# Optimization experiments

Hardware: AMD Instinct MI355X
Metric: run time of the kernel (lower is better)

## Reference

```python
import jax, jax.numpy as jnp
import numpy as np

NUM_CLASSES = 2
THRESH = 0.5        # overlap_thresh
NEGPOS = 3          # neg:pos ratio
VAR = (0.1, 0.2)    # cfg['variance']
B, P, O = 64, 32768, 50


def point_form(p):
    # center-size [cx,cy,w,h] -> corner [xmin,ymin,xmax,ymax]
    return jnp.concatenate([p[:, :2] - p[:, 2:] * 0.5, p[:, :2] + p[:, 2:] * 0.5], axis=1)


def iou(a, b):
    # a [O,4], b [P,4] corner form -> [O,P]
    lt = jnp.maximum(a[:, None, :2], b[None, :, :2])
    rb = jnp.minimum(a[:, None, 2:], b[None, :, 2:])
    wh = jnp.clip(rb - lt, 0.0, None)
    inter = wh[..., 0] * wh[..., 1]
    area_a = ((a[:, 2] - a[:, 0]) * (a[:, 3] - a[:, 1]))[:, None]
    area_b = ((b[:, 2] - b[:, 0]) * (b[:, 3] - b[:, 1]))[None, :]
    return inter / (area_a + area_b - inter)


def encode(matched, priors_cs):
    g_cxcy = ((matched[:, :2] + matched[:, 2:]) * 0.5 - priors_cs[:, :2]) / (VAR[0] * priors_cs[:, 2:])
    g_wh = jnp.log((matched[:, 2:] - matched[:, :2]) / priors_cs[:, 2:]) / VAR[1]
    return jnp.concatenate([g_cxcy, g_wh], axis=1)


def match_one(truths, labels, priors_cs, priors_pt):
    ovl = iou(truths, priors_pt)                # [O,P]
    best_prior_idx = jnp.argmax(ovl, axis=1)    # [O] best prior per GT
    best_truth_ovl = jnp.max(ovl, axis=0)       # [P]
    best_truth_idx = jnp.argmax(ovl, axis=0)    # [P]
    best_truth_ovl = best_truth_ovl.at[best_prior_idx].set(2.0)
    best_truth_idx = best_truth_idx.at[best_prior_idx].set(jnp.arange(truths.shape[0]))
    matched = truths[best_truth_idx]            # [P,4]
    conf = jnp.where(best_truth_ovl < THRESH, 0, labels[best_truth_idx])
    return encode(matched, priors_cs), conf


def reference(arm_loc, arm_conf, odm_loc, odm_conf, priors, targets):
    loc_data, conf_data = arm_loc, arm_conf    # use_ARM=False -> ARM branch
    num, num_priors = loc_data.shape[0], loc_data.shape[1]
    truths = targets[..., :4]
    labels = (targets[..., 4] >= 0).astype(jnp.int32)   # num_classes == 2 binarization
    priors_pt = point_form(priors)
    loc_t, conf_t = jax.vmap(lambda t, l: match_one(t, l, priors, priors_pt))(truths, labels)
    loc_t = jax.lax.stop_gradient(loc_t)
    conf_t = jax.lax.stop_gradient(conf_t)
    pos = conf_t > 0                             # [B,P]
    # localization: smooth L1, summed over positives
    d = loc_data - loc_t
    ad = jnp.abs(d)
    sl1 = jnp.where(ad < 1.0, 0.5 * d * d, ad - 0.5)
    loss_l = jnp.sum(sl1 * pos[..., None].astype(loc_data.dtype))
    # per-prior conf loss for hard negative mining
    lse = jax.nn.logsumexp(conf_data, axis=-1)   # [B,P]
    picked = jnp.take_along_axis(conf_data, conf_t[..., None], axis=-1)[..., 0]
    lc = lse - picked                            # NLL per prior
    lc_mine = jnp.where(pos, 0.0, lc)            # zero positives before ranking
    order = jnp.argsort(-lc_mine, axis=1)        # descending sort
    rank = jnp.argsort(order, axis=1)            # rank of each prior
    num_pos = jnp.sum(pos, axis=1, keepdims=True)            # [B,1]
    num_neg = jnp.minimum(NEGPOS * num_pos, num_priors - 1)
    neg = rank < num_neg
    sel = (pos | neg).astype(conf_data.dtype)
    loss_c = jnp.sum(lc * sel)
    N = jnp.sum(num_pos).astype(loc_data.dtype)
    return loss_l / N, loss_c / N


def setup_inputs():
    key = jax.random.key(0)
    ks = jax.random.split(key, 8)
    arm_loc = jax.random.normal(ks[0], (B, P, 4), jnp.float32)
    arm_conf = jax.random.normal(ks[1], (B, P, NUM_CLASSES), jnp.float32)
    odm_loc = jax.random.normal(ks[2], (B, P, 4), jnp.float32)
    odm_conf = jax.random.normal(ks[3], (B, P, NUM_CLASSES), jnp.float32)
    # priors in center-size form
    p_cxcy = jax.random.uniform(ks[4], (P, 2), jnp.float32, 0.05, 0.95)
    p_wh = jax.random.uniform(ks[5], (P, 2), jnp.float32, 0.05, 0.5)
    priors = jnp.concatenate([p_cxcy, p_wh], axis=1)
    # GT boxes in corner form with valid extents, labels >= 0
    t_cxcy = jax.random.uniform(ks[6], (B, O, 2), jnp.float32, 0.2, 0.8)
    t_wh = jax.random.uniform(ks[7], (B, O, 2), jnp.float32, 0.05, 0.3)
    boxes = jnp.concatenate([t_cxcy - t_wh * 0.5, t_cxcy + t_wh * 0.5], axis=-1)
    targets = jnp.concatenate([boxes, jnp.ones((B, O, 1), jnp.float32)], axis=-1)
    return {"arm_loc": arm_loc, "arm_conf": arm_conf, "odm_loc": odm_loc,
            "odm_conf": odm_conf, "priors": priors, "targets": targets}
```

## Files before the change

kernel.cpp:

```cpp
#include <hip/hip_runtime.h>
#include <cstdint>

#pragma clang fp contract(off)

#define BB 64
#define PP 32768
#define OO 50
#define THRESH_F 0.5f
#define VAR0 0.1f
#define VAR1 0.2f
#define NEGPOS_I 3
#define SS 32
#define T1 4
#define NB0 2048
#define NB12 1024
#define NCELL 1024

typedef unsigned long long u64;

__device__ __forceinline__ unsigned mpart4(unsigned x) {
    x = (x | (x << 2)) & 0x33u;
    x = (x | (x << 1)) & 0x55u;
    return x;
}
__device__ __forceinline__ int cell_of(float4 pr) {
    int xb = (int)(pr.x * 16.0f); xb = xb < 0 ? 0 : (xb > 15 ? 15 : xb);
    int yb = (int)(pr.y * 16.0f); yb = yb < 0 ? 0 : (yb > 15 ? 15 : yb);
    float s = fmaxf(pr.z, pr.w);
    int wc = s < 0.275f ? 0 : (s < 0.368f ? 1 : (s < 0.44f ? 2 : 3));
    return wc * 256 + (int)(mpart4((unsigned)xb) | (mpart4((unsigned)yb) << 1));
}

__global__ void k_zero(float4* __restrict__ dst, int n4) {
    int i = blockIdx.x * blockDim.x + threadIdx.x;
    if (i < n4) dst[i] = make_float4(0.f, 0.f, 0.f, 0.f);
}

__global__ void k_phist(const float4* __restrict__ pri, int* __restrict__ cnt) {
    int p = blockIdx.x * 1024 + threadIdx.x * 4;
    for (int j = 0; j < 4; ++j)
        atomicAdd(&cnt[cell_of(pri[p + j])], 1);
}

__global__ void __launch_bounds__(256)
k_pss(const float4* __restrict__ pri, const int* __restrict__ cnt,
      int* __restrict__ cursor, int* __restrict__ perm, int* __restrict__ iperm) {
    __shared__ int sc[256];
    __shared__ int sbase[NCELL];
    int tid = threadIdx.x;
    int a[4]; int s = 0;
    for (int i = 0; i < 4; ++i) { a[i] = cnt[tid * 4 + i]; s += a[i]; }
    sc[tid] = s; __syncthreads();
    for (int off = 1; off < 256; off <<= 1) {
        int v = (tid >= off) ? sc[tid - off] : 0;
        __syncthreads(); sc[tid] += v; __syncthreads();
    }
    int excl = sc[tid] - s;
    for (int i = 0; i < 4; ++i) { sbase[tid * 4 + i] = excl; excl += a[i]; }
    __syncthreads();
    int p = blockIdx.x * 1024 + tid * 4;
    for (int j = 0; j < 4; ++j) {
        int c = cell_of(pri[p + j]);
        int pos = sbase[c] + atomicAdd(&cursor[c], 1);
        perm[pos] = p + j;
        iperm[p + j] = pos;
    }
}

#define DPP_MAX(x, ctrl, rmask)                                              \
    {                                                                        \
        int _o = __float_as_int(x);                                          \
        x = fmaxf(x, __int_as_float(__builtin_amdgcn_update_dpp(             \
                _o, _o, (ctrl), (rmask), 0xf, false)));                      \
    }
#define DPP_MINF(x, ctrl, rmask)                                             \
    {                                                                        \
        int _o = __float_as_int(x);                                          \
        x = fminf(x, __int_as_float(__builtin_amdgcn_update_dpp(             \
                _o, _o, (ctrl), (rmask), 0xf, false)));                      \
    }
#define WAVE_MAXF(x) { DPP_MAX(x,0x111,0xf); DPP_MAX(x,0x112,0xf); DPP_MAX(x,0x114,0xf); \
                       DPP_MAX(x,0x118,0xf); DPP_MAX(x,0x142,0xa); DPP_MAX(x,0x143,0xc); }
#define WAVE_MINF(x) { DPP_MINF(x,0x111,0xf); DPP_MINF(x,0x112,0xf); DPP_MINF(x,0x114,0xf); \
                       DPP_MINF(x,0x118,0xf); DPP_MINF(x,0x142,0xa); DPP_MINF(x,0x143,0xc); }

__device__ __forceinline__ float sl1enc(const float* __restrict__ tb,
                                        float4 pr, float4 ld) {
    float gx = ((tb[0] + tb[2]) * 0.5f - pr.x) / (VAR0 * pr.z);
    float gy = ((tb[1] + tb[3]) * 0.5f - pr.y) / (VAR0 * pr.w);
    float gw = logf((tb[2] - tb[0]) / pr.z) / VAR1;
    float gh = logf((tb[3] - tb[1]) / pr.w) / VAR1;
    float g[4] = {gx, gy, gw, gh};
    float l[4] = {ld.x, ld.y, ld.z, ld.w};
    float s = 0.f;
    for (int q = 0; q < 4; ++q) {
        float d = l[q] - g[q];
        float ad = fabsf(d);
        s += (ad < 1.0f) ? 0.5f * d * d : ad - 0.5f;
    }
    return s;
}

__global__ void __launch_bounds__(256, 8)
k_ml(const float* __restrict__ priors, const int* __restrict__ perm,
     const float* __restrict__ targets,
     const float* __restrict__ arm_loc, const float* __restrict__ arm_conf,
     float* __restrict__ lcmP, unsigned char* __restrict__ bpiP,
     u64* __restrict__ bpm,
     float* __restrict__ pll, float* __restrict__ pplc, int* __restrict__ pnp) {
    __shared__ float4 trP[OO];
    __shared__ float2 trQ[OO];
    __shared__ float s1[256]; __shared__ float s2[256]; __shared__ int s3[256];
    int b = (blockIdx.x % 8) * 8 + (blockIdx.y % 8);
    int s = (blockIdx.x / 8) + 4 * (blockIdx.y / 8);
    int tid = threadIdx.x;
    if (tid < OO) {
        const float* tb = &targets[(size_t)(b * OO + tid) * 5];
        float x0 = tb[0], y0 = tb[1], x1 = tb[2], y1 = tb[3];
        trP[tid] = make_float4(x0, y0, x1, y1);
        trQ[tid] = make_float2((x1 - x0) * (y1 - y0), tb[4]);
    }
    __syncthreads();

    int p0 = s * (256 * T1) + tid * T1;
    int4 o4 = ((const int4*)perm)[p0 >> 2];
    int o_[T1] = {o4.x, o4.y, o4.z, o4.w};
    int omin = min(min(o_[0], o_[1]), min(o_[2], o_[3]));
    float bx0[T1], by0[T1], bx1[T1], by1[T1], aB[T1];
#pragma unroll
    for (int j = 0; j < T1; ++j) {
        float4 pr = ((const float4*)priors)[o_[j]];
        bx0[j] = pr.x - pr.z * 0.5f; by0[j] = pr.y - pr.w * 0.5f;
        bx1[j] = pr.x + pr.z * 0.5f; by1[j] = pr.y + pr.w * 0.5f;
        aB[j] = (bx1[j] - bx0[j]) * (by1[j] - by0[j]);
    }
    float lx0 = fminf(fminf(bx0[0], bx0[1]), fminf(bx0[2], bx0[3]));
    float ly0 = fminf(fminf(by0[0], by0[1]), fminf(by0[2], by0[3]));
    float lx1 = fmaxf(fmaxf(bx1[0], bx1[1]), fmaxf(bx1[2], bx1[3]));
    float ly1 = fmaxf(fmaxf(by1[0], by1[1]), fmaxf(by1[2], by1[3]));
    WAVE_MINF(lx0); WAVE_MINF(ly0); WAVE_MAXF(lx1); WAVE_MAXF(ly1);
    float wx0 = __int_as_float(__builtin_amdgcn_readlane(__float_as_int(lx0), 63));
    float wy0 = __int_as_float(__builtin_amdgcn_readlane(__float_as_int(ly0), 63));
    float wx1 = __int_as_float(__builtin_amdgcn_readlane(__float_as_int(lx1), 63));
    float wy1 = __int_as_float(__builtin_amdgcn_readlane(__float_as_int(ly1), 63));

    float rbv[T1]; int rbi[T1];
#pragma unroll
    for (int j = 0; j < T1; ++j) { rbv[j] = 0.0f; rbi[j] = 0; }

    for (int t = 0; t < OO; ++t) {
        float4 tP = trP[t];
        if (!(tP.z > wx0 && tP.x < wx1 && tP.w > wy0 && tP.y < wy1)) continue;
        float aA = trQ[t].x;
        float I[T1];
#pragma unroll
        for (int j = 0; j < T1; ++j) {
            float ltx = fmaxf(tP.x, bx0[j]), lty = fmaxf(tP.y, by0[j]);
            float rbx = fminf(tP.z, bx1[j]), rby = fminf(tP.w, by1[j]);
            float wx = fmaxf(rbx - ltx, 0.f), wy = fmaxf(rby - lty, 0.f);
            I[j] = wx * wy;
        }
        bool anyl = (I[0] > 0.f) | (I[1] > 0.f) | (I[2] > 0.f) | (I[3] > 0.f);
        if (__any(anyl)) {
            float cbv = 0.0f; int cbo = omin;
#pragma unroll
            for (int j = 0; j < T1; ++j) {
                float v = I[j] / (aA + aB[j] - I[j]);
                if (v > rbv[j]) { rbv[j] = v; rbi[j] = t; }
                if (v > cbv || (v == cbv && o_[j] < cbo)) { cbv = v; cbo = o_[j]; }
            }
            float x = cbv;
            WAVE_MAXF(x);
            float mvf = __int_as_float(__builtin_amdgcn_readlane(__float_as_int(x), 63));
            if (mvf > 0.0f) {
                u64 msk = __ballot(cbv == mvf);
                int ln = (int)__ffsll((long long)msk) - 1;
                int morig = __builtin_amdgcn_readlane(cbo, ln);
                u64 rest = msk & (msk - 1);
                while (rest) {
                    int l2 = (int)__ffsll((long long)rest) - 1;
                    int o2 = __builtin_amdgcn_readlane(cbo, l2);
                    morig = min(morig, o2);
                    rest &= rest - 1;
                }
                if ((tid & 63) == 0) {
                    u64 pk = ((u64)__float_as_uint(mvf) << 32) | (unsigned)(PP - morig);
                    atomicMax(&bpm[b * OO + t], pk);
                }
            }
        }
    }

    size_t bbase = (size_t)b * PP;
    float ll = 0.0f, plc = 0.0f; int np = 0;
    float outv[4]; unsigned pbyte = 0;
#pragma unroll
    for (int c = 0; c < T1; ++c) {
        int o = o_[c]; size_t bo = bbase + o;
        int ti = rbi[c]; float ov = rbv[c];
        float2 cf = ((const float2*)arm_conf)[bo];
        float c0 = cf.x, c1 = cf.y;
        float m = fmaxf(c0, c1);
        float lse = logf(expf(c0 - m) + expf(c1 - m)) + m;
        bool pos = (ov >= THRESH_F) && (trQ[ti].y >= 0.0f);
        float lc = lse - (pos ? c1 : c0);
        outv[c] = pos ? 0.0f : lc;
        pbyte |= (unsigned)((pos ? 0x80u : 0u) | (unsigned)ti) << (8 * c);
        if (pos) {
            np++; plc += lc;
            float4 pr = ((const float4*)priors)[o];
            float4 ld = ((const float4*)arm_loc)[bo];
            const float4 tv = trP[ti];
            float tb4[4] = {tv.x, tv.y, tv.z, tv.w};
            ll += sl1enc(tb4, pr, ld);
        }
    }
    size_t bq = bbase + p0;
    ((float4*)lcmP)[bq >> 2] = make_float4(outv[0], outv[1], outv[2], outv[3]);
    ((unsigned*)bpiP)[bq >> 2] = pbyte;

    s1[tid] = ll; s2[tid] = plc; s3[tid] = np;
    __syncthreads();
    for (int st = 128; st > 0; st >>= 1) {
        if (tid < st) { s1[tid] += s1[tid+st]; s2[tid] += s2[tid+st]; s3[tid] += s3[tid+st]; }
        __syncthreads();
    }
    if (tid == 0) {
        pll[s * BB + b] = s1[0];
        pplc[s * BB + b] = s2[0];
        pnp[s * BB + b] = s3[0];
    }
}

__global__ void k_fix(const u64* __restrict__ bpm, const float* __restrict__ targets,
                      const float* __restrict__ arm_loc, const float* __restrict__ arm_conf,
                      const float* __restrict__ priors, const int* __restrict__ iperm,
                      const unsigned char* __restrict__ bpiP, float* __restrict__ lcmP,
                      float* __restrict__ pll, float* __restrict__ pplc,
                      int* __restrict__ pnp, int* __restrict__ npb) {
    int b = blockIdx.x, j = threadIdx.x;
    int p = -1;
    if (j < OO) {
        unsigned lo = (unsigned)(bpm[b * OO + j] & 0xFFFFFFFFull);
        p = lo ? (PP - (int)lo) : 0;
    }
    bool w = (j < OO);
    for (int jj = 1; jj < OO; ++jj) {
        int pj = __shfl(p, jj, 64);
        if (jj > j && pj == p) w = false;
    }
    float dll = 0.f, dplc = 0.f; int dnp = 0;
    if (w) {
        int pos_ = iperm[p];
        size_t bq = (size_t)b * PP + pos_;
        size_t bo = (size_t)b * PP + p;
        unsigned char ob = bpiP[bq];
        bool old_pos = (ob & 0x80u) != 0;
        int old_ti = ob & 63;
        float2 cf = ((const float2*)arm_conf)[bo];
        float c0 = cf.x, c1 = cf.y;
        float m = fmaxf(c0, c1);
        float lse = logf(expf(c0 - m) + expf(c1 - m)) + m;
        const float* tbj = &targets[(size_t)(b * OO + j) * 5];
        bool new_pos = (tbj[4] >= 0.0f);
        float new_lcm = new_pos ? 0.0f : (lse - c0);
        lcmP[bq] = new_lcm;
        float4 pr = ((const float4*)priors)[p];
        float4 ld = ((const float4*)arm_loc)[bo];
        if (old_pos) {
            dnp -= 1; dplc -= (lse - c1);
            dll -= sl1enc(&targets[(size_t)(b * OO + old_ti) * 5], pr, ld);
        }
        if (new_pos) {
            dnp += 1; dplc += (lse - c1);
            dll += sl1enc(tbj, pr, ld);
        }
    }
    int myp = (j < SS) ? pnp[j * BB + b] : 0;
    for (int st = 32; st >= 1; st >>= 1) {
        dll += __shfl_down(dll, st, 64);
        dplc += __shfl_down(dplc, st, 64);
        dnp += __shfl_down(dnp, st, 64);
        myp += __shfl_down(myp, st, 64);
    }
    if (j == 0) {
        pll[b] += dll;
        pplc[b] += dplc;
        pnp[b] += dnp;
        npb[b] = myp + dnp;
    }
}

__global__ void __launch_bounds__(256)
k_sel(const float* __restrict__ lcmP, const int* __restrict__ npb,
      float* __restrict__ ssum, int* __restrict__ srem, unsigned* __restrict__ stb) {
    __shared__ int hc[NB0]; __shared__ float hs[NB0];
    __shared__ int sc[256]; __shared__ float sf[256];
    __shared__ int s_chunk, s_r; __shared__ float s_S; __shared__ unsigned s_pref;
    int b = blockIdx.x, tid = threadIdx.x;
    const float4* v4 = (const float4*)(lcmP + (size_t)b * PP);

    {
        for (int i = tid; i < NB0; i += 256) { hc[i] = 0; hs[i] = 0.f; }
        __syncthreads();
        for (int it = 0; it < 32; ++it) {
            float4 x = v4[it * 256 + tid];
            float xs[4] = {x.x, x.y, x.z, x.w};
            for (int c2 = 0; c2 < 4; ++c2) {
                unsigned u = __float_as_uint(xs[c2]);
                atomicAdd(&hc[u >> 20], 1);
                atomicAdd(&hs[u >> 20], xs[c2]);
            }
        }
        __syncthreads();
        int c = 0; float f = 0.f; int base = tid * 8;
        for (int i = 0; i < 8; ++i) { c += hc[base + i]; f += hs[base + i]; }
        sc[tid] = c; sf[tid] = f;
        if (tid == 0) {
            int k = NEGPOS_I * npb[b]; if (k > PP - 1) k = PP - 1;
            s_r = k; s_S = 0.f;
        }
        __syncthreads();
        for (int off = 1; off < 256; off <<= 1) {
            int cv = (tid + off < 256) ? sc[tid + off] : 0;
            float fv = (tid + off < 256) ? sf[tid + off] : 0.f;
            __syncthreads(); sc[tid] += cv; sf[tid] += fv; __syncthreads();
        }
        int r = s_r;
        int nxt = (tid == 255) ? 0 : sc[tid + 1];
        if (sc[tid] >= r && nxt < r) s_chunk = tid;
        __syncthreads();
        if (tid == 0) {
            int ch = s_chunk;
            int r2 = r - ((ch == 255) ? 0 : sc[ch + 1]);
            float S2 = s_S + ((ch == 255) ? 0.f : sf[ch + 1]);
            int binSel = ch * 8;
            for (int i = 7; i >= 0; --i) {
                int bin = ch * 8 + i; int cbn = hc[bin];
                if (r2 <= cbn) { binSel = bin; break; }
                r2 -= cbn; S2 += hs[bin];
            }
            s_pref = (unsigned)binSel; s_r = r2; s_S = S2;
        }
        __syncthreads();
    }
    {
        for (int i = tid; i < NB12; i += 256) { hc[i] = 0; hs[i] = 0.f; }
        __syncthreads();
        unsigned pref = s_pref;
        for (int it = 0; it < 32; ++it) {
            float4 x = v4[it * 256 + tid];
            float xs[4] = {x.x, x.y, x.z, x.w};
            for (int c2 = 0; c2 < 4; ++c2) {
                unsigned u = __float_as_uint(xs[c2]);
                if ((u >> 20) == pref) {
                    atomicAdd(&hc[(u >> 10) & 1023u], 1);
                    atomicAdd(&hs[(u >> 10) & 1023u], xs[c2]);
                }
            }
        }
        __syncthreads();
        int c = 0; float f = 0.f; int base = tid * 4;
        for (int i = 0; i < 4; ++i) { c += hc[base + i]; f += hs[base + i]; }
        sc[tid] = c; sf[tid] = f; __syncthreads();
        for (int off = 1; off < 256; off <<= 1) {
            int cv = (tid + off < 256) ? sc[tid + off] : 0;
            float fv = (tid + off < 256) ? sf[tid + off] : 0.f;
            __syncthreads(); sc[tid] += cv; sf[tid] += fv; __syncthreads();
        }
        int r = s_r;
        int nxt = (tid == 255) ? 0 : sc[tid + 1];
        if (sc[tid] >= r && nxt < r) s_chunk = tid;
        __syncthreads();
        if (tid == 0) {
            int ch = s_chunk;
            int r2 = r - ((ch == 255) ? 0 : sc[ch + 1]);
            float S2 = s_S + ((ch == 255) ? 0.f : sf[ch + 1]);
            int binSel = ch * 4;
            for (int i = 3; i >= 0; --i) {
                int bin = ch * 4 + i; int cbn = hc[bin];
                if (r2 <= cbn) { binSel = bin; break; }
                r2 -= cbn; S2 += hs[bin];
            }
            s_pref = (s_pref << 10) | (unsigned)binSel; s_r = r2; s_S = S2;
        }
        __syncthreads();
    }
    {
        for (int i = tid; i < NB12; i += 256) { hc[i] = 0; hs[i] = 0.f; }
        __syncthreads();
        unsigned pref = s_pref;
        for (int it = 0; it < 32; ++it) {
            float4 x = v4[it * 256 + tid];
            float xs[4] = {x.x, x.y, x.z, x.w};
            for (int c2 = 0; c2 < 4; ++c2) {
                unsigned u = __float_as_uint(xs[c2]);
                if ((u >> 10) == pref) {
                    atomicAdd(&hc[u & 1023u], 1);
                    atomicAdd(&hs[u & 1023u], xs[c2]);
                }
            }
        }
        __syncthreads();
        int c = 0; float f = 0.f; int base = tid * 4;
        for (int i = 0; i < 4; ++i) { c += hc[base + i]; f += hs[base + i]; }
        sc[tid] = c; sf[tid] = f; __syncthreads();
        for (int off = 1; off < 256; off <<= 1) {
            int cv = (tid + off < 256) ? sc[tid + off] : 0;
            float fv = (tid + off < 256) ? sf[tid + off] : 0.f;
            __syncthreads(); sc[tid] += cv; sf[tid] += fv; __syncthreads();
        }
        int r = s_r;
        int nxt = (tid == 255) ? 0 : sc[tid + 1];
        if (sc[tid] >= r && nxt < r) s_chunk = tid;
        __syncthreads();
        if (tid == 0) {
            int ch = s_chunk;
            int r2 = r - ((ch == 255) ? 0 : sc[ch + 1]);
            float S2 = s_S + ((ch == 255) ? 0.f : sf[ch + 1]);
            int binSel = ch * 4;
            for (int i = 3; i >= 0; --i) {
                int bin = ch * 4 + i; int cbn = hc[bin];
                if (r2 <= cbn) { binSel = bin; break; }
                r2 -= cbn; S2 += hs[bin];
            }
            stb[b] = (s_pref << 10) | (unsigned)binSel;
            srem[b] = r2; ssum[b] = S2;
        }
    }
}

__global__ void k_final(const float* __restrict__ pll, const float* __restrict__ pplc,
                        const int* __restrict__ pnp, const float* __restrict__ ssum,
                        const int* __restrict__ srem, const unsigned* __restrict__ stb,
                        float* __restrict__ out) {
    int b = threadIdx.x;
    float ll = 0.f, plc = 0.f; int np = 0;
    for (int s = 0; s < SS; ++s) {
        ll += pll[s * BB + b];
        plc += pplc[s * BB + b];
        np += pnp[s * BB + b];
    }
    float tval = __uint_as_float(stb[b]);
    float cc = plc + ssum[b] + (float)srem[b] * tval;
    for (int s = 32; s > 0; s >>= 1) {
        ll += __shfl_down(ll, s);
        cc += __shfl_down(cc, s);
        np += __shfl_down(np, s);
    }
    if (b == 0) {
        float N = (float)np;
        out[0] = ll / N;
        out[1] = cc / N;
    }
}

extern "C" void kernel_launch(void* const* d_in, const int* in_sizes, int n_in,
                              void* d_out, int out_size, void* d_ws, size_t ws_size,
                              hipStream_t stream) {
    const float* arm_loc  = (const float*)d_in[0];
    const float* arm_conf = (const float*)d_in[1];
    const float* priors   = (const float*)d_in[4];
    const float* targets  = (const float*)d_in[5];
    float* out = (float*)d_out;

    char* w = (char*)d_ws;
    float* lcmP = (float*)w;  w += sizeof(float) * (size_t)BB * PP;
    unsigned char* bpiP = (unsigned char*)w; w += (size_t)BB * PP;
    char* zbase = w;
    int*   cellCnt = (int*)w; w += sizeof(int) * NCELL;
    int*   cursor  = (int*)w; w += sizeof(int) * NCELL;
    u64*   bpm = (u64*)w;    w += sizeof(u64)   * BB * OO;
    size_t zbytes = (size_t)(w - zbase);
    int*   perm  = (int*)w;  w += sizeof(int) * PP;
    int*   iperm = (int*)w;  w += sizeof(int) * PP;
    float* pll  = (float*)w; w += sizeof(float) * BB * SS;
    float* pplc = (float*)w; w += sizeof(float) * BB * SS;
    int*   pnp  = (int*)w;   w += sizeof(int)   * BB * SS;
    int*   npb  = (int*)w;   w += sizeof(int)   * BB;
    int*      srem = (int*)w;      w += sizeof(int) * BB;
    float*    ssum = (float*)w;    w += sizeof(float) * BB;
    unsigned* stb  = (unsigned*)w; w += sizeof(unsigned) * BB;

    int n4 = (int)(zbytes / 16);
    k_zero<<<(n4 + 255) / 256, 256, 0, stream>>>((float4*)zbase, n4);
    k_phist<<<PP / 1024, 256, 0, stream>>>((const float4*)priors, cellCnt);
    k_pss<<<PP / 1024, 256, 0, stream>>>((const float4*)priors, cellCnt, cursor, perm, iperm);
    k_ml<<<dim3(SS, BB), 256, 0, stream>>>(priors, perm, targets, arm_loc, arm_conf,
                                           lcmP, bpiP, bpm, pll, pplc, pnp);
    k_fix<<<BB, 64, 0, stream>>>(bpm, targets, arm_loc, arm_conf, priors, iperm,
                                 bpiP, lcmP, pll, pplc, pnp, npb);
    k_sel<<<BB, 256, 0, stream>>>(lcmP, npb, ssum, srem, stb);
    k_final<<<1, 64, 0, stream>>>(pll, pplc, pnp, ssum, srem, stb, out);
}
```

Measured before the change: 304.5 us.

## Build first radix-select histogram in match kernel and merge prior-sort kernels

The match kernel now builds a per-batch 256-bin histogram (count and sum) over the float exponent bits of the negative-loss values, using shared-memory atomics that are then flushed to global memory. The fix kernel patches this histogram whenever it changes a value. The selection kernel uses the precomputed histogram as its first radix pass, so only two full passes over the loss array remain instead of three, with 12-bit and 11-bit digits. The prior-cell counting sort is merged into a single 1024-thread block kernel, removing one launch and the global atomics, at the cost of running serially on one CU and adding atomic traffic inside the match kernel.

```diff
diff --git a/kernel.cpp b/kernel.cpp
--- a/kernel.cpp
+++ b/kernel.cpp
@@ -12,8 +12,9 @@
 #define NEGPOS_I 3
 #define SS 32
 #define T1 4
-#define NB0 2048
-#define NB12 1024
+#define NB_P0 256
+#define NB_P1 4096
+#define NB_P2 2048
 #define NCELL 1024
 
 typedef unsigned long long u64;
@@ -36,34 +37,30 @@
     if (i < n4) dst[i] = make_float4(0.f, 0.f, 0.f, 0.f);
 }
 
-__global__ void k_phist(const float4* __restrict__ pri, int* __restrict__ cnt) {
-    int p = blockIdx.x * 1024 + threadIdx.x * 4;
-    for (int j = 0; j < 4; ++j)
-        atomicAdd(&cnt[cell_of(pri[p + j])], 1);
-}
-
-__global__ void __launch_bounds__(256)
-k_pss(const float4* __restrict__ pri, const int* __restrict__ cnt,
-      int* __restrict__ cursor, int* __restrict__ perm, int* __restrict__ iperm) {
-    __shared__ int sc[256];
-    __shared__ int sbase[NCELL];
+__global__ void __launch_bounds__(1024)
+k_prep(const float4* __restrict__ pri, int* __restrict__ perm, int* __restrict__ iperm) {
+    __shared__ int cnt[NCELL];
+    __shared__ int tmp[NCELL];
     int tid = threadIdx.x;
-    int a[4]; int s = 0;
-    for (int i = 0; i < 4; ++i) { a[i] = cnt[tid * 4 + i]; s += a[i]; }
-    sc[tid] = s; __syncthreads();
-    for (int off = 1; off < 256; off <<= 1) {
-        int v = (tid >= off) ? sc[tid - off] : 0;
-        __syncthreads(); sc[tid] += v; __syncthreads();
-    }
-    int excl = sc[tid] - s;
-    for (int i = 0; i < 4; ++i) { sbase[tid * 4 + i] = excl; excl += a[i]; }
-    __syncthreads();
-    int p = blockIdx.x * 1024 + tid * 4;
-    for (int j = 0; j < 4; ++j) {
-        int c = cell_of(pri[p + j]);
-        int pos = sbase[c] + atomicAdd(&cursor[c], 1);
-        perm[pos] = p + j;
-        iperm[p + j] = pos;
+    cnt[tid] = 0;
+    __syncthreads();
+    for (int i = 0; i < 32; ++i)
+        atomicAdd(&cnt[cell_of(pri[i * 1024 + tid])], 1);
+    __syncthreads();
+    int v = cnt[tid]; tmp[tid] = v;
+    __syncthreads();
+    for (int off = 1; off < 1024; off <<= 1) {
+        int a = (tid >= off) ? tmp[tid - off] : 0;
+        __syncthreads(); tmp[tid] += a; __syncthreads();
+    }
+    cnt[tid] = tmp[tid] - v;
+    __syncthreads();
+    for (int i = 0; i < 32; ++i) {
+        int p = i * 1024 + tid;
+        int c = cell_of(pri[p]);
+        int pos = atomicAdd(&cnt[c], 1);
+        perm[pos] = p;
+        iperm[p] = pos;
     }
 }
 
@@ -107,9 +104,12 @@
      const float* __restrict__ arm_loc, const float* __restrict__ arm_conf,
      float* __restrict__ lcmP, unsigned char* __restrict__ bpiP,
      u64* __restrict__ bpm,
-     float* __restrict__ pll, float* __restrict__ pplc, int* __restrict__ pnp) {
+     float* __restrict__ pll, float* __restrict__ pplc, int* __restrict__ pnp,
+     int* __restrict__ Hc0, float* __restrict__ Hs0) {
     __shared__ float4 trP[OO];
     __shared__ float2 trQ[OO];
+    __shared__ int   hc[NB_P0];
+    __shared__ float hs[NB_P0];
     __shared__ float s1[256]; __shared__ float s2[256]; __shared__ int s3[256];
     int b = (blockIdx.x % 8) * 8 + (blockIdx.y % 8);
     int s = (blockIdx.x / 8) + 4 * (blockIdx.y / 8);
@@ -120,6 +120,7 @@
         trP[tid] = make_float4(x0, y0, x1, y1);
         trQ[tid] = make_float2((x1 - x0) * (y1 - y0), tb[4]);
     }
+    hc[tid] = 0; hs[tid] = 0.f;
     __syncthreads();
 
     int p0 = s * (256 * T1) + tid * T1;
@@ -206,6 +207,9 @@
         float lc = lse - (pos ? c1 : c0);
         outv[c] = pos ? 0.0f : lc;
         pbyte |= (unsigned)((pos ? 0x80u : 0u) | (unsigned)ti) << (8 * c);
+        unsigned u = __float_as_uint(outv[c]);
+        atomicAdd(&hc[u >> 23], 1);
+        atomicAdd(&hs[u >> 23], outv[c]);
         if (pos) {
             np++; plc += lc;
             float4 pr = ((const float4*)priors)[o];
@@ -219,6 +223,14 @@
     ((float4*)lcmP)[bq >> 2] = make_float4(outv[0], outv[1], outv[2], outv[3]);
     ((unsigned*)bpiP)[bq >> 2] = pbyte;
 
+    __syncthreads();
+    {
+        int cv = hc[tid];
+        if (cv) {
+            atomicAdd(&Hc0[b * NB_P0 + tid], cv);
+            atomicAdd(&Hs0[b * NB_P0 + tid], hs[tid]);
+        }
+    }
     s1[tid] = ll; s2[tid] = plc; s3[tid] = np;
     __syncthreads();
     for (int st = 128; st > 0; st >>= 1) {
@@ -237,7 +249,8 @@
                       const float* __restrict__ priors, const int* __restrict__ iperm,
                       const unsigned char* __restrict__ bpiP, float* __restrict__ lcmP,
                       float* __restrict__ pll, float* __restrict__ pplc,
-                      int* __restrict__ pnp, int* __restrict__ npb) {
+                      int* __restrict__ pnp, int* __restrict__ npb,
+                      int* __restrict__ Hc0, float* __restrict__ Hs0) {
     int b = blockIdx.x, j = threadIdx.x;
     int p = -1;
     if (j < OO) {
@@ -263,8 +276,16 @@
         float lse = logf(expf(c0 - m) + expf(c1 - m)) + m;
         const float* tbj = &targets[(size_t)(b * OO + j) * 5];
         bool new_pos = (tbj[4] >= 0.0f);
+        float old_lcm = lcmP[bq];
         float new_lcm = new_pos ? 0.0f : (lse - c0);
-        lcmP[bq] = new_lcm;
+        unsigned uo = __float_as_uint(old_lcm), un = __float_as_uint(new_lcm);
+        if (uo != un) {
+            atomicAdd(&Hc0[b * NB_P0 + (uo >> 23)], -1);
+            atomicAdd(&Hs0[b * NB_P0 + (uo >> 23)], -old_lcm);
+            atomicAdd(&Hc0[b * NB_P0 + (un >> 23)], 1);
+            atomicAdd(&Hs0[b * NB_P0 + (un >> 23)], new_lcm);
+            lcmP[bq] = new_lcm;
+        }
         float4 pr = ((const float4*)priors)[p];
         float4 ld = ((const float4*)arm_loc)[bo];
         if (old_pos) {
@@ -293,34 +314,101 @@
 
 __global__ void __launch_bounds__(256)
 k_sel(const float* __restrict__ lcmP, const int* __restrict__ npb,
+      const int* __restrict__ Hc0, const float* __restrict__ Hs0,
       float* __restrict__ ssum, int* __restrict__ srem, unsigned* __restrict__ stb) {
-    __shared__ int hc[NB0]; __shared__ float hs[NB0];
+    __shared__ int hc[NB_P1]; __shared__ float hs[NB_P1];
     __shared__ int sc[256]; __shared__ float sf[256];
     __shared__ int s_chunk, s_r; __shared__ float s_S; __shared__ unsigned s_pref;
     int b = blockIdx.x, tid = threadIdx.x;
     const float4* v4 = (const float4*)(lcmP + (size_t)b * PP);
 
     {
-        for (int i = tid; i < NB0; i += 256) { hc[i] = 0; hs[i] = 0.f; }
-        __syncthreads();
+        int c = Hc0[b * NB_P0 + tid];
+        float f = Hs0[b * NB_P0 + tid];
+        sc[tid] = c; sf[tid] = f;
+        if (tid == 0) {
+            int k = NEGPOS_I * npb[b]; if (k > PP - 1) k = PP - 1;
+            s_r = k; s_S = 0.f;
+        }
+        __syncthreads();
+        for (int off = 1; off < 256; off <<= 1) {
+            int cv = (tid + off < 256) ? sc[tid + off] : 0;
+            float fv = (tid + off < 256) ? sf[tid + off] : 0.f;
+            __syncthreads(); sc[tid] += cv; sf[tid] += fv; __syncthreads();
+        }
+        int r = s_r;
+        int nxt = (tid == 255) ? 0 : sc[tid + 1];
+        if (sc[tid] >= r && nxt < r) s_chunk = tid;
+        __syncthreads();
+        if (tid == 0) {
+            int ch = s_chunk;
+            s_pref = (unsigned)ch;
+            s_r = r - ((ch == 255) ? 0 : sc[ch + 1]);
+            s_S = (ch == 255) ? 0.f : sf[ch + 1];
+        }
+        __syncthreads();
+    }
+    {
+        for (int i = tid; i < NB_P1; i += 256) { hc[i] = 0; hs[i] = 0.f; }
+        __syncthreads();
+        unsigned pref = s_pref;
         for (int it = 0; it < 32; ++it) {
             float4 x = v4[it * 256 + tid];
             float xs[4] = {x.x, x.y, x.z, x.w};
             for (int c2 = 0; c2 < 4; ++c2) {
                 unsigned u = __float_as_uint(xs[c2]);
-                atomicAdd(&hc[u >> 20], 1);
-                atomicAdd(&hs[u >> 20], xs[c2]);
+                if ((u >> 23) == pref) {
+                    atomicAdd(&hc[(u >> 11) & 4095u], 1);
+                    atomicAdd(&hs[(u >> 11) & 4095u], xs[c2]);
+                }
+            }
+        }
+        __syncthreads();
+        int c = 0; float f = 0.f; int base = tid * 16;
+        for (int i = 0; i < 16; ++i) { c += hc[base + i]; f += hs[base + i]; }
+        sc[tid] = c; sf[tid] = f; __syncthreads();
+        for (int off = 1; off < 256; off <<= 1) {
+            int cv = (tid + off < 256) ? sc[tid + off] : 0;
+            float fv = (tid + off < 256) ? sf[tid + off] : 0.f;
+            __syncthreads(); sc[tid] += cv; sf[tid] += fv; __syncthreads();
+        }
+        int r = s_r;
+        int nxt = (tid == 255) ? 0 : sc[tid + 1];
+        if (sc[tid] >= r && nxt < r) s_chunk = tid;
+        __syncthreads();
+        if (tid == 0) {
+            int ch = s_chunk;
+            int r2 = r - ((ch == 255) ? 0 : sc[ch + 1]);
+            float S2 = s_S + ((ch == 255) ? 0.f : sf[ch + 1]);
+            int binSel = ch * 16;
+            for (int i = 15; i >= 0; --i) {
+                int bin = ch * 16 + i; int cbn = hc[bin];
+                if (r2 <= cbn) { binSel = bin; break; }
+                r2 -= cbn; S2 += hs[bin];
+            }
+            s_pref = (s_pref << 12) | (unsigned)binSel; s_r = r2; s_S = S2;
+        }
+        __syncthreads();
+    }
+    {
+        for (int i = tid; i < NB_P2; i += 256) { hc[i] = 0; hs[i] = 0.f; }
+        __syncthreads();
+        unsigned pref = s_pref;
+        for (int it = 0; it < 32; ++it) {
+            float4 x = v4[it * 256 + tid];
+            float xs[4] = {x.x, x.y, x.z, x.w};
+            for (int c2 = 0; c2 < 4; ++c2) {
+                unsigned u = __float_as_uint(xs[c2]);
+                if ((u >> 11) == pref) {
+                    atomicAdd(&hc[u & 2047u], 1);
+                    atomicAdd(&hs[u & 2047u], xs[c2]);
+                }
             }
         }
         __syncthreads();
         int c = 0; float f = 0.f; int base = tid * 8;
         for (int i = 0; i < 8; ++i) { c += hc[base + i]; f += hs[base + i]; }
-        sc[tid] = c; sf[tid] = f;
-        if (tid == 0) {
-            int k = NEGPOS_I * npb[b]; if (k > PP - 1) k = PP - 1;
-            s_r = k; s_S = 0.f;
-        }
-        __syncthreads();
+        sc[tid] = c; sf[tid] = f; __syncthreads();
         for (int off = 1; off < 256; off <<= 1) {
             int cv = (tid + off < 256) ? sc[tid + off] : 0;
             float fv = (tid + off < 256) ? sf[tid + off] : 0.f;
@@ -340,91 +428,7 @@
                 if (r2 <= cbn) { binSel = bin; break; }
                 r2 -= cbn; S2 += hs[bin];
             }
-            s_pref = (unsigned)binSel; s_r = r2; s_S = S2;
-        }
-        __syncthreads();
-    }
-    {
-        for (int i = tid; i < NB12; i += 256) { hc[i] = 0; hs[i] = 0.f; }
-        __syncthreads();
-        unsigned pref = s_pref;
-        for (int it = 0; it < 32; ++it) {
-            float4 x = v4[it * 256 + tid];
-            float xs[4] = {x.x, x.y, x.z, x.w};
-            for (int c2 = 0; c2 < 4; ++c2) {
-                unsigned u = __float_as_uint(xs[c2]);
-                if ((u >> 20) == pref) {
-                    atomicAdd(&hc[(u >> 10) & 1023u], 1);
-                    atomicAdd(&hs[(u >> 10) & 1023u], xs[c2]);
-                }
-            }
-        }
-        __syncthreads();
-        int c = 0; float f = 0.f; int base = tid * 4;
-        for (int i = 0; i < 4; ++i) { c += hc[base + i]; f += hs[base + i]; }
-        sc[tid] = c; sf[tid] = f; __syncthreads();
-        for (int off = 1; off < 256; off <<= 1) {
-            int cv = (tid + off < 256) ? sc[tid + off] : 0;
-            float fv = (tid + off < 256) ? sf[tid + off] : 0.f;
-            __syncthreads(); sc[tid] += cv; sf[tid] += fv; __syncthreads();
-        }
-        int r = s_r;
-        int nxt = (tid == 255) ? 0 : sc[tid + 1];
-        if (sc[tid] >= r && nxt < r) s_chunk = tid;
-        __syncthreads();
-        if (tid == 0) {
-            int ch = s_chunk;
-            int r2 = r - ((ch == 255) ? 0 : sc[ch + 1]);
-            float S2 = s_S + ((ch == 255) ? 0.f : sf[ch + 1]);
-            int binSel = ch * 4;
-            for (int i = 3; i >= 0; --i) {
-                int bin = ch * 4 + i; int cbn = hc[bin];
-                if (r2 <= cbn) { binSel = bin; break; }
-                r2 -= cbn; S2 += hs[bin];
-            }
-            s_pref = (s_pref << 10) | (unsigned)binSel; s_r = r2; s_S = S2;
-        }
-        __syncthreads();
-    }
-    {
-        for (int i = tid; i < NB12; i += 256) { hc[i] = 0; hs[i] = 0.f; }
-        __syncthreads();
-        unsigned pref = s_pref;
-        for (int it = 0; it < 32; ++it) {
-            float4 x = v4[it * 256 + tid];
-            float xs[4] = {x.x, x.y, x.z, x.w};
-            for (int c2 = 0; c2 < 4; ++c2) {
-                unsigned u = __float_as_uint(xs[c2]);
-                if ((u >> 10) == pref) {
-                    atomicAdd(&hc[u & 1023u], 1);
-                    atomicAdd(&hs[u & 1023u], xs[c2]);
-                }
-            }
-        }
-        __syncthreads();
-        int c = 0; float f = 0.f; int base = tid * 4;
-        for (int i = 0; i < 4; ++i) { c += hc[base + i]; f += hs[base + i]; }
-        sc[tid] = c; sf[tid] = f; __syncthreads();
-        for (int off = 1; off < 256; off <<= 1) {
-            int cv = (tid + off < 256) ? sc[tid + off] : 0;
-            float fv = (tid + off < 256) ? sf[tid + off] : 0.f;
-            __syncthreads(); sc[tid] += cv; sf[tid] += fv; __syncthreads();
-        }
-        int r = s_r;
-        int nxt = (tid == 255) ? 0 : sc[tid + 1];
-        if (sc[tid] >= r && nxt < r) s_chunk = tid;
-        __syncthreads();
-        if (tid == 0) {
-            int ch = s_chunk;
-            int r2 = r - ((ch == 255) ? 0 : sc[ch + 1]);
-            float S2 = s_S + ((ch == 255) ? 0.f : sf[ch + 1]);
-            int binSel = ch * 4;
-            for (int i = 3; i >= 0; --i) {
-                int bin = ch * 4 + i; int cbn = hc[bin];
-                if (r2 <= cbn) { binSel = bin; break; }
-                r2 -= cbn; S2 += hs[bin];
-            }
-            stb[b] = (s_pref << 10) | (unsigned)binSel;
+            stb[b] = (s_pref << 11) | (unsigned)binSel;
             srem[b] = r2; ssum[b] = S2;
         }
     }
@@ -468,8 +472,8 @@
     float* lcmP = (float*)w;  w += sizeof(float) * (size_t)BB * PP;
     unsigned char* bpiP = (unsigned char*)w; w += (size_t)BB * PP;
     char* zbase = w;
-    int*   cellCnt = (int*)w; w += sizeof(int) * NCELL;
-    int*   cursor  = (int*)w; w += sizeof(int) * NCELL;
+    int*   Hc0 = (int*)w;    w += sizeof(int)   * BB * NB_P0;
+    float* Hs0 = (float*)w;  w += sizeof(float) * BB * NB_P0;
     u64*   bpm = (u64*)w;    w += sizeof(u64)   * BB * OO;
     size_t zbytes = (size_t)(w - zbase);
     int*   perm  = (int*)w;  w += sizeof(int) * PP;
@@ -484,12 +488,11 @@
 
     int n4 = (int)(zbytes / 16);
     k_zero<<<(n4 + 255) / 256, 256, 0, stream>>>((float4*)zbase, n4);
-    k_phist<<<PP / 1024, 256, 0, stream>>>((const float4*)priors, cellCnt);
-    k_pss<<<PP / 1024, 256, 0, stream>>>((const float4*)priors, cellCnt, cursor, perm, iperm);
+    k_prep<<<1, 1024, 0, stream>>>((const float4*)priors, perm, iperm);
     k_ml<<<dim3(SS, BB), 256, 0, stream>>>(priors, perm, targets, arm_loc, arm_conf,
-                                           lcmP, bpiP, bpm, pll, pplc, pnp);
+                                           lcmP, bpiP, bpm, pll, pplc, pnp, Hc0, Hs0);
     k_fix<<<BB, 64, 0, stream>>>(bpm, targets, arm_loc, arm_conf, priors, iperm,
-                                 bpiP, lcmP, pll, pplc, pnp, npb);
-    k_sel<<<BB, 256, 0, stream>>>(lcmP, npb, ssum, srem, stb);
+                                 bpiP, lcmP, pll, pplc, pnp, npb, Hc0, Hs0);
+    k_sel<<<BB, 256, 0, stream>>>(lcmP, npb, Hc0, Hs0, ssum, srem, stb);
     k_final<<<1, 64, 0, stream>>>(pll, pplc, pnp, ssum, srem, stb, out);
 }
```

Measured after the change: 289.6 us. 1.05x faster.
